# Kernel tuning notes

Measured on AMD Instinct MI355X. Metric: run time of the kernel, lower is better.

Reference implementation:

```python
import jax, jax.numpy as jnp
import numpy as np

DIM = 128
HEADS = 4
WIN = (2, 7, 7)
SHIFT = (1, 3, 3)
B, D, H, W = 8, 8, 56, 56
LN_EPS = 1e-5


def _rel_pos_index(ws):
    # static (N, N) int index into the relative position bias table
    coords = np.stack(np.meshgrid(np.arange(ws[0]), np.arange(ws[1]), np.arange(ws[2]), indexing='ij'))
    cf = coords.reshape(3, -1)
    rel = (cf[:, :, None] - cf[:, None, :]).transpose(1, 2, 0)  # (N, N, 3)
    rel[:, :, 0] += ws[0] - 1
    rel[:, :, 1] += ws[1] - 1
    rel[:, :, 2] += ws[2] - 1
    rel[:, :, 0] *= (2 * ws[1] - 1) * (2 * ws[2] - 1)
    rel[:, :, 1] *= 2 * ws[2] - 1
    return rel.sum(-1)


_REL_IDX = _rel_pos_index(WIN)  # (98, 98)


def _layernorm(x, g, b):
    m = x.mean(-1, keepdims=True)
    v = ((x - m) ** 2).mean(-1, keepdims=True)
    return (x - m) * jax.lax.rsqrt(v + LN_EPS) * g + b


def _forward(x, mask_matrix, norm1_g, norm1_b, qkv_w, qkv_b, rel_bias,
             proj_w, proj_b, norm2_g, norm2_b, fc1_w, fc1_b, fc2_w, fc2_b):
    Bx, Dx, Hx, Wx, C = x.shape
    wd, wh, ww = WIN
    sd, sh, sw = SHIFT
    N = wd * wh * ww
    hd = C // HEADS

    shortcut = x
    h = _layernorm(x, norm1_g, norm1_b)
    # cyclic shift (D, H, W divisible by window -> no padding needed)
    h = jnp.roll(h, (-sd, -sh, -sw), axis=(1, 2, 3))
    # window partition -> (B_, N, C)
    xw = h.reshape(Bx, Dx // wd, wd, Hx // wh, wh, Wx // ww, ww, C)
    xw = xw.transpose(0, 1, 3, 5, 2, 4, 6, 7).reshape(-1, N, C)
    B_ = xw.shape[0]

    qkv = xw @ qkv_w.T + qkv_b  # (B_, N, 3C)
    qkv = qkv.reshape(B_, N, 3, HEADS, hd).transpose(2, 0, 3, 1, 4)  # (3, B_, h, N, hd)
    q = qkv[0] * (hd ** -0.5)
    k = qkv[1]
    v = qkv[2]

    attn = jnp.einsum('bhnd,bhmd->bhnm', q, k)  # (B_, h, N, N)
    bias = rel_bias[_REL_IDX.reshape(-1)].reshape(N, N, HEADS).transpose(2, 0, 1)
    attn = attn + bias[None]
    nW = mask_matrix.shape[0]
    attn = attn.reshape(B_ // nW, nW, HEADS, N, N) + mask_matrix[None, :, None]
    attn = jax.nn.softmax(attn.reshape(B_, HEADS, N, N), axis=-1)

    out = jnp.einsum('bhnm,bhmd->bnhd', attn, v).reshape(B_, N, C)
    out = out @ proj_w.T + proj_b
    # window reverse -> (B, D, H, W, C)
    out = out.reshape(Bx, Dx // wd, Hx // wh, Wx // ww, wd, wh, ww, C)
    out = out.transpose(0, 1, 4, 2, 5, 3, 6, 7).reshape(Bx, Dx, Hx, Wx, C)
    out = jnp.roll(out, (sd, sh, sw), axis=(1, 2, 3))

    x = shortcut + out
    y = _layernorm(x, norm2_g, norm2_b)
    y = jax.nn.gelu(y @ fc1_w.T + fc1_b, approximate=False)
    y = y @ fc2_w.T + fc2_b
    return x + y


def setup_inputs():
    key = jax.random.key(0)
    ks = jax.random.split(key, 6)
    C = DIM
    wd, wh, ww = WIN
    x = jax.random.normal(ks[0], (B, D, H, W, C), jnp.float32)

    # shifted-window attention mask (standard Video-Swin compute_mask)
    img_mask = np.zeros((1, D, H, W, 1), np.float32)
    cnt = 0
    sl = lambda w, s: (slice(0, -w), slice(-w, -s), slice(-s, None))
    for d in sl(WIN[0], SHIFT[0]):
        for h in sl(WIN[1], SHIFT[1]):
            for w in sl(WIN[2], SHIFT[2]):
                img_mask[:, d, h, w, :] = cnt
                cnt += 1
    mw = img_mask.reshape(1, D // wd, wd, H // wh, wh, W // ww, ww, 1)
    mw = mw.transpose(0, 1, 3, 5, 2, 4, 6, 7).reshape(-1, wd * wh * ww)  # (nW, N)
    am = mw[:, None, :] - mw[:, :, None]
    mask_matrix = jnp.asarray(np.where(am != 0, -100.0, 0.0).astype(np.float32))

    nbias = (2 * wd - 1) * (2 * wh - 1) * (2 * ww - 1)
    p = lambda k, shape: jax.random.normal(k, shape, jnp.float32) * 0.02
    return {
        'x': x, 'mask_matrix': mask_matrix,
        'norm1_g': jnp.ones((C,), jnp.float32), 'norm1_b': jnp.zeros((C,), jnp.float32),
        'qkv_w': p(ks[1], (3 * C, C)), 'qkv_b': jnp.zeros((3 * C,), jnp.float32),
        'rel_bias': p(ks[2], (nbias, HEADS)),
        'proj_w': p(ks[3], (C, C)), 'proj_b': jnp.zeros((C,), jnp.float32),
        'norm2_g': jnp.ones((C,), jnp.float32), 'norm2_b': jnp.zeros((C,), jnp.float32),
        'fc1_w': p(ks[4], (4 * C, C)), 'fc1_b': jnp.zeros((4 * C,), jnp.float32),
        'fc2_w': p(ks[5], (C, 4 * C)), 'fc2_b': jnp.zeros((C,), jnp.float32),
    }


def reference(x, mask_matrix, norm1_g, norm1_b, qkv_w, qkv_b, rel_bias,
              proj_w, proj_b, norm2_g, norm2_b, fc1_w, fc1_b, fc2_w, fc2_b):
    return _forward(x, mask_matrix, norm1_g, norm1_b, qkv_w, qkv_b, rel_bias,
                    proj_w, proj_b, norm2_g, norm2_b, fc1_w, fc1_b, fc2_w, fc2_b)
```

## Files before the change

kernel.cpp:

```cpp
#include <hip/hip_runtime.h>
#include <hip/hip_bf16.h>

#define C_DIM 128
#define N_WIN 98
#define M_TOK 200704
#define B_WIN 2048

struct __align__(8) bf16x4 { __hip_bfloat16 h[4]; };

typedef __attribute__((ext_vector_type(8))) short bf16x8_t;
typedef __attribute__((ext_vector_type(4))) float f32x4_t;

__device__ __forceinline__ int token_spatial_index(int row) {
    int widx = row / 98;
    int n = row - widx * 98;
    int b   = widx >> 8;
    int rem = widx & 255;
    int dI = rem >> 6;
    int hI = (rem >> 3) & 7;
    int wI = rem & 7;
    int dw = n / 49;
    int r49 = n - dw * 49;
    int hw = r49 / 7;
    int ww = r49 - hw * 7;
    int d = dI * 2 + dw;
    int h = hI * 7 + hw;
    int w = wI * 7 + ww;
    d = (d + 1) & 7;
    h += 3; if (h >= 56) h -= 56;
    w += 3; if (w >= 56) w -= 56;
    return ((b * 8 + d) * 56 + h) * 56 + w;
}

__global__ __launch_bounds__(256) void ln1_qkv_kernel(
    const float* __restrict__ x,
    const float* __restrict__ g1,
    const float* __restrict__ b1,
    const float* __restrict__ qkv_w,
    const float* __restrict__ qkv_b,
    __hip_bfloat16* __restrict__ qkv_out)
{
    __shared__ __align__(16) __hip_bfloat16 Abf[64][136];
    __shared__ __align__(16) __hip_bfloat16 Wbf[192][136];
    __shared__ int srcL[64];

    const int tid  = threadIdx.x;
    const int lane = tid & 63;
    const int wv   = tid >> 6;
    const int rowbase = blockIdx.x * 64;

    if (tid < 64) srcL[tid] = token_spatial_index(rowbase + tid);
    __syncthreads();

    {
        int r = tid >> 2, part = tid & 3;
        const float* xp = x + (size_t)srcL[r] * 128 + part * 32;
        float v[32];
        float s = 0.f, ss = 0.f;
        #pragma unroll
        for (int j = 0; j < 8; ++j) {
            float4 f = *(const float4*)(xp + j * 4);
            v[j*4+0] = f.x; v[j*4+1] = f.y; v[j*4+2] = f.z; v[j*4+3] = f.w;
            s  += f.x + f.y + f.z + f.w;
            ss += f.x*f.x + f.y*f.y + f.z*f.z + f.w*f.w;
        }
        s += __shfl_xor(s, 1); ss += __shfl_xor(ss, 1);
        s += __shfl_xor(s, 2); ss += __shfl_xor(ss, 2);
        float m = s * (1.f / 128.f);
        float var = ss * (1.f / 128.f) - m * m;
        float rstd = rsqrtf(var + 1e-5f);
        #pragma unroll
        for (int j = 0; j < 8; ++j) {
            int k = part * 32 + j * 4;
            bf16x4 pk;
            pk.h[0] = __float2bfloat16((v[j*4+0] - m) * rstd * g1[k+0] + b1[k+0]);
            pk.h[1] = __float2bfloat16((v[j*4+1] - m) * rstd * g1[k+1] + b1[k+1]);
            pk.h[2] = __float2bfloat16((v[j*4+2] - m) * rstd * g1[k+2] + b1[k+2]);
            pk.h[3] = __float2bfloat16((v[j*4+3] - m) * rstd * g1[k+3] + b1[k+3]);
            *(bf16x4*)(&Abf[r][k]) = pk;
        }
    }
    __syncthreads();

    const int lm = lane & 15, quad = lane >> 4;
    const int rw = wv * 16;

    bf16x8_t xfr[4];
    #pragma unroll
    for (int s = 0; s < 4; ++s)
        xfr[s] = *(const bf16x8_t*)(&Abf[rw + lm][s * 32 + quad * 8]);

    for (int nt = 0; nt < 2; ++nt) {
        #pragma unroll
        for (int i = 0; i < 24; ++i) {
            int e = tid + i * 256;
            int c = e >> 5, kq = e & 31;
            float4 f = *(const float4*)(qkv_w + (size_t)(nt * 192 + c) * 128 + kq * 4);
            bf16x4 pk;
            pk.h[0] = __float2bfloat16(f.x); pk.h[1] = __float2bfloat16(f.y);
            pk.h[2] = __float2bfloat16(f.z); pk.h[3] = __float2bfloat16(f.w);
            *(bf16x4*)(&Wbf[c][kq * 4]) = pk;
        }
        __syncthreads();

        for (int ct = 0; ct < 12; ++ct) {
            f32x4_t acc = {0.f, 0.f, 0.f, 0.f};
            #pragma unroll
            for (int s = 0; s < 4; ++s) {
                bf16x8_t wfr = *(const bf16x8_t*)(&Wbf[ct * 16 + lm][s * 32 + quad * 8]);
                acc = __builtin_amdgcn_mfma_f32_16x16x32_bf16(wfr, xfr[s], acc, 0, 0, 0);
            }
            int grow = rowbase + rw + lm;
            int gcol = nt * 192 + ct * 16 + quad * 4;
            float4 bb = *(const float4*)(qkv_b + gcol);
            bf16x4 pk;
            pk.h[0] = __float2bfloat16(acc[0] + bb.x);
            pk.h[1] = __float2bfloat16(acc[1] + bb.y);
            pk.h[2] = __float2bfloat16(acc[2] + bb.z);
            pk.h[3] = __float2bfloat16(acc[3] + bb.w);
            *(bf16x4*)(qkv_out + (size_t)grow * 384 + gcol) = pk;
        }
        __syncthreads();
    }
}

__global__ __launch_bounds__(256) void attn_mfma_kernel(
    __hip_bfloat16* __restrict__ qkv,
    const float* __restrict__ rel_bias)
{
    __shared__ __align__(16) __hip_bfloat16 Qb[112][40];
    __shared__ __align__(16) __hip_bfloat16 Kb[112][40];
    __shared__ __align__(16) __hip_bfloat16 Vt[32][136];
    __shared__ __align__(16) __hip_bfloat16 Pb[112][136];
    __shared__ float biasL[507];
    __shared__ int   idn[98];

    const int tid  = threadIdx.x;
    const int lane = tid & 63;
    const int wv   = tid >> 6;
    const int widx = blockIdx.x >> 2;
    const int head = blockIdx.x & 3;
    const int co   = head * 32;
    const size_t base = (size_t)widx * 98 * 384;

    bf16x8_t zz = {};
    for (int e = tid; e < 448; e += 256) {
        int row = e >> 2, c8 = e & 3;
        if (row < 98) {
            size_t g = base + (size_t)row * 384;
            *(bf16x8_t*)(&Qb[row][c8 * 8]) = *(const bf16x8_t*)(qkv + g + co + c8 * 8);
            *(bf16x8_t*)(&Kb[row][c8 * 8]) = *(const bf16x8_t*)(qkv + g + 128 + co + c8 * 8);
        } else {
            *(bf16x8_t*)(&Qb[row][c8 * 8]) = zz;
            *(bf16x8_t*)(&Kb[row][c8 * 8]) = zz;
        }
    }
    for (int e = tid; e < 448; e += 256) {
        int row = e >> 2, c8 = e & 3;
        if (row < 98) {
            bf16x8_t v = *(const bf16x8_t*)(qkv + base + (size_t)row * 384 + 256 + co + c8 * 8);
            #pragma unroll
            for (int j = 0; j < 8; ++j) Vt[c8 * 8 + j][row] = ((__hip_bfloat16*)&v)[j];
        }
    }
    for (int e = tid; e < 1024; e += 256) {
        int r = e >> 5, c = 96 + (e & 31);
        if (c >= 98) Vt[r][c] = __float2bfloat16(0.f);
    }
    for (int e = tid; e < 1792; e += 256) {
        int r = e >> 4, c = 112 + (e & 15);
        Pb[r][c] = __float2bfloat16(0.f);
    }
    for (int i = tid; i < 507; i += 256) biasL[i] = rel_bias[i * 4 + head];
    if (tid < 98) {
        int wloc = widx & 255;
        int dI = wloc >> 6, hI = (wloc >> 3) & 7, wI = wloc & 7;
        int n = tid;
        int dw = n / 49, r49 = n - dw * 49, hw = r49 / 7, ww2 = r49 - hw * 7;
        int d = dI * 2 + dw, h = hI * 7 + hw, w = wI * 7 + ww2;
        int di = (d < 6) ? 0 : (d < 7 ? 1 : 2);
        int hi = (h < 49) ? 0 : (h < 52 ? 1 : 2);
        int wi = (w < 49) ? 0 : (w < 52 ? 1 : 2);
        idn[n] = di * 9 + hi * 3 + wi;
    }
    __syncthreads();

    const int lm = lane & 15, quad = lane >> 4;
    const float scale = 0.17677669529663687f;

    for (int tM = wv; tM < 7; tM += 4) {
        bf16x8_t afr = *(const bf16x8_t*)(&Qb[tM * 16 + lm][quad * 8]);
        f32x4_t acc[7];
        #pragma unroll
        for (int tN = 0; tN < 7; ++tN) {
            bf16x8_t bfr = *(const bf16x8_t*)(&Kb[tN * 16 + lm][quad * 8]);
            f32x4_t c0 = {0.f, 0.f, 0.f, 0.f};
            acc[tN] = __builtin_amdgcn_mfma_f32_16x16x32_bf16(afr, bfr, c0, 0, 0, 0);
        }
        float sv[7][4];
        #pragma unroll
        for (int tN = 0; tN < 7; ++tN) {
            int m = tN * 16 + lm;
            #pragma unroll
            for (int rg = 0; rg < 4; ++rg) {
                int n = tM * 16 + quad * 4 + rg;
                float s;
                if (n < 98 && m < 98) {
                    int d1 = n / 49, r1 = n - d1 * 49, h1 = r1 / 7, w1 = r1 - h1 * 7;
                    int d2 = m / 49, r2 = m - d2 * 49, h2 = r2 / 7, w2 = r2 - h2 * 7;
                    int bidx = (d1 - d2 + 1) * 169 + (h1 - h2 + 6) * 13 + (w1 - w2 + 6);
                    s = acc[tN][rg] * scale + biasL[bidx];
                    s += (idn[n] == idn[m]) ? 0.f : -100.f;
                } else {
                    s = -1e30f;
                }
                sv[tN][rg] = s;
            }
        }
        #pragma unroll
        for (int rg = 0; rg < 4; ++rg) {
            float mx = sv[0][rg];
            #pragma unroll
            for (int tN = 1; tN < 7; ++tN) mx = fmaxf(mx, sv[tN][rg]);
            mx = fmaxf(mx, __shfl_xor(mx, 1));
            mx = fmaxf(mx, __shfl_xor(mx, 2));
            mx = fmaxf(mx, __shfl_xor(mx, 4));
            mx = fmaxf(mx, __shfl_xor(mx, 8));
            float p[7], sum = 0.f;
            #pragma unroll
            for (int tN = 0; tN < 7; ++tN) { p[tN] = __expf(sv[tN][rg] - mx); sum += p[tN]; }
            sum += __shfl_xor(sum, 1);
            sum += __shfl_xor(sum, 2);
            sum += __shfl_xor(sum, 4);
            sum += __shfl_xor(sum, 8);
            float inv = 1.f / sum;
            int n = tM * 16 + quad * 4 + rg;
            #pragma unroll
            for (int tN = 0; tN < 7; ++tN)
                Pb[n][tN * 16 + lm] = __float2bfloat16(p[tN] * inv);
        }
    }
    __syncthreads();

    for (int t = wv; t < 14; t += 4) {
        int tM = t >> 1, tN = t & 1;
        f32x4_t acc = {0.f, 0.f, 0.f, 0.f};
        #pragma unroll
        for (int s = 0; s < 4; ++s) {
            bf16x8_t afr = *(const bf16x8_t*)(&Pb[tM * 16 + lm][s * 32 + quad * 8]);
            bf16x8_t bfr = *(const bf16x8_t*)(&Vt[tN * 16 + lm][s * 32 + quad * 8]);
            acc = __builtin_amdgcn_mfma_f32_16x16x32_bf16(afr, bfr, acc, 0, 0, 0);
        }
        int m = tN * 16 + lm;
        #pragma unroll
        for (int rg = 0; rg < 4; ++rg) {
            int n = tM * 16 + quad * 4 + rg;
            if (n < 98)
                qkv[base + (size_t)n * 384 + co + m] = __float2bfloat16(acc[rg]);
        }
    }
}

__global__ __launch_bounds__(256) void proj_kernel(
    const __hip_bfloat16* __restrict__ attn,
    const float* __restrict__ proj_w,
    const float* __restrict__ proj_b,
    const float* __restrict__ x,
    float* __restrict__ x2)
{
    __shared__ __align__(16) __hip_bfloat16 Abf[64][136];
    __shared__ __align__(16) __hip_bfloat16 Wbf[128][136];
    __shared__ int dstL[64];

    const int tid  = threadIdx.x;
    const int lane = tid & 63;
    const int wv   = tid >> 6;
    const int rowbase = blockIdx.x * 64;

    if (tid < 64) dstL[tid] = token_spatial_index(rowbase + tid);

    #pragma unroll
    for (int i = 0; i < 4; ++i) {
        int e = tid + i * 256;
        int r = e >> 4, c8 = e & 15;
        *(bf16x8_t*)(&Abf[r][c8 * 8]) = *(const bf16x8_t*)(attn + (size_t)(rowbase + r) * 384 + c8 * 8);
    }
    #pragma unroll
    for (int i = 0; i < 16; ++i) {
        int e = tid + i * 256;
        int c = e >> 5, kq = e & 31;
        float4 f = *(const float4*)(proj_w + (size_t)c * 128 + kq * 4);
        bf16x4 pk;
        pk.h[0] = __float2bfloat16(f.x); pk.h[1] = __float2bfloat16(f.y);
        pk.h[2] = __float2bfloat16(f.z); pk.h[3] = __float2bfloat16(f.w);
        *(bf16x4*)(&Wbf[c][kq * 4]) = pk;
    }
    __syncthreads();

    const int lm = lane & 15, quad = lane >> 4;
    const int rw = wv * 16;

    bf16x8_t xfr[4];
    #pragma unroll
    for (int s = 0; s < 4; ++s)
        xfr[s] = *(const bf16x8_t*)(&Abf[rw + lm][s * 32 + quad * 8]);

    const int dst = dstL[rw + lm];

    #pragma unroll
    for (int ct = 0; ct < 8; ++ct) {
        f32x4_t acc = {0.f, 0.f, 0.f, 0.f};
        #pragma unroll
        for (int s = 0; s < 4; ++s) {
            bf16x8_t wfr = *(const bf16x8_t*)(&Wbf[ct * 16 + lm][s * 32 + quad * 8]);
            acc = __builtin_amdgcn_mfma_f32_16x16x32_bf16(wfr, xfr[s], acc, 0, 0, 0);
        }
        int gcol = ct * 16 + quad * 4;
        float4 bb = *(const float4*)(proj_b + gcol);
        size_t off = (size_t)dst * 128 + gcol;
        float4 xr = *(const float4*)(x + off);
        float4 res;
        res.x = acc[0] + bb.x + xr.x;
        res.y = acc[1] + bb.y + xr.y;
        res.z = acc[2] + bb.z + xr.z;
        res.w = acc[3] + bb.w + xr.w;
        *(float4*)(x2 + off) = res;
    }
}

__global__ __launch_bounds__(256) void prep_weights(
    const float* __restrict__ fc1_w,
    const float* __restrict__ fc2_w,
    __hip_bfloat16* __restrict__ wb)
{
    int i = blockIdx.x * 256 + threadIdx.x;
    if (i < 65536)       wb[i] = __float2bfloat16(fc1_w[i]);
    else if (i < 131072) wb[i] = __float2bfloat16(fc2_w[i - 65536]);
}

__global__ __launch_bounds__(256, 3) void mlp_mfma_kernel(
    const float* __restrict__ x2,
    const float* __restrict__ g2,
    const float* __restrict__ b2,
    const __hip_bfloat16* __restrict__ fc1_wb,
    const __hip_bfloat16* __restrict__ fc2_wb,
    const float* __restrict__ fc1_b,
    const float* __restrict__ fc2_b,
    float* __restrict__ out)
{
    __shared__ __align__(16) __hip_bfloat16 Abf[64][136];
    __shared__ __align__(16) __hip_bfloat16 Hbf[64][264];

    const int tid  = threadIdx.x;
    const int lane = tid & 63;
    const int wv   = tid >> 6;
    const int rowbase = blockIdx.x * 64;

    {
        int r = tid >> 2, part = tid & 3;
        const float* xp = x2 + (size_t)(rowbase + r) * 128 + part * 32;
        float v[32];
        float s = 0.f, ss = 0.f;
        #pragma unroll
        for (int j = 0; j < 8; ++j) {
            float4 f = *(const float4*)(xp + j * 4);
            v[j*4+0] = f.x; v[j*4+1] = f.y; v[j*4+2] = f.z; v[j*4+3] = f.w;
            s  += f.x + f.y + f.z + f.w;
            ss += f.x*f.x + f.y*f.y + f.z*f.z + f.w*f.w;
        }
        s += __shfl_xor(s, 1); ss += __shfl_xor(ss, 1);
        s += __shfl_xor(s, 2); ss += __shfl_xor(ss, 2);
        float m = s * (1.f / 128.f);
        float var = ss * (1.f / 128.f) - m * m;
        float rstd = rsqrtf(var + 1e-5f);
        #pragma unroll
        for (int j = 0; j < 8; ++j) {
            int k = part * 32 + j * 4;
            bf16x4 pk;
            pk.h[0] = __float2bfloat16((v[j*4+0] - m) * rstd * g2[k+0] + b2[k+0]);
            pk.h[1] = __float2bfloat16((v[j*4+1] - m) * rstd * g2[k+1] + b2[k+1]);
            pk.h[2] = __float2bfloat16((v[j*4+2] - m) * rstd * g2[k+2] + b2[k+2]);
            pk.h[3] = __float2bfloat16((v[j*4+3] - m) * rstd * g2[k+3] + b2[k+3]);
            *(bf16x4*)(&Abf[r][k]) = pk;
        }
    }
    __syncthreads();

    const int lm   = lane & 15;
    const int quad = lane >> 4;

    f32x4_t acc2[2][4];
    #pragma unroll
    for (int ct = 0; ct < 2; ++ct)
        #pragma unroll
        for (int rt = 0; rt < 4; ++rt)
            acc2[ct][rt] = f32x4_t{0.f, 0.f, 0.f, 0.f};

    for (int c = 0; c < 2; ++c) {
        {
            bf16x8_t afr[4][4];
            #pragma unroll
            for (int rt = 0; rt < 4; ++rt)
                #pragma unroll
                for (int s = 0; s < 4; ++s)
                    afr[rt][s] = *(const bf16x8_t*)(&Abf[rt * 16 + lm][s * 32 + quad * 8]);

            #pragma unroll
            for (int ctb = 0; ctb < 2; ++ctb) {
                bf16x8_t wfr[2][4];
                #pragma unroll
                for (int cti = 0; cti < 2; ++cti) {
                    int hcol = c * 256 + wv * 64 + (ctb * 2 + cti) * 16 + lm;
                    const __hip_bfloat16* wp = fc1_wb + (size_t)hcol * 128 + quad * 8;
                    #pragma unroll
                    for (int s = 0; s < 4; ++s)
                        wfr[cti][s] = *(const bf16x8_t*)(wp + s * 32);
                }
                #pragma unroll
                for (int cti = 0; cti < 2; ++cti) {
                    int ct = ctb * 2 + cti;
                    int hcol = c * 256 + wv * 64 + ct * 16 + lm;
                    float bb = fc1_b[hcol];
                    f32x4_t a0 = {0.f,0.f,0.f,0.f}, a1 = {0.f,0.f,0.f,0.f};
                    f32x4_t a2 = {0.f,0.f,0.f,0.f}, a3 = {0.f,0.f,0.f,0.f};
                    #pragma unroll
                    for (int s = 0; s < 4; ++s) {
                        a0 = __builtin_amdgcn_mfma_f32_16x16x32_bf16(afr[0][s], wfr[cti][s], a0, 0, 0, 0);
                        a1 = __builtin_amdgcn_mfma_f32_16x16x32_bf16(afr[1][s], wfr[cti][s], a1, 0, 0, 0);
                        a2 = __builtin_amdgcn_mfma_f32_16x16x32_bf16(afr[2][s], wfr[cti][s], a2, 0, 0, 0);
                        a3 = __builtin_amdgcn_mfma_f32_16x16x32_bf16(afr[3][s], wfr[cti][s], a3, 0, 0, 0);
                    }
                    int lc = wv * 64 + ct * 16 + lm;
                    #pragma unroll
                    for (int rg = 0; rg < 4; ++rg) {
                        float v0 = a0[rg] + bb, v1 = a1[rg] + bb, v2 = a2[rg] + bb, v3 = a3[rg] + bb;
                        v0 = 0.5f * v0 * (1.f + erff(v0 * 0.70710678118654752f));
                        v1 = 0.5f * v1 * (1.f + erff(v1 * 0.70710678118654752f));
                        v2 = 0.5f * v2 * (1.f + erff(v2 * 0.70710678118654752f));
                        v3 = 0.5f * v3 * (1.f + erff(v3 * 0.70710678118654752f));
                        Hbf[ 0 + quad * 4 + rg][lc] = __float2bfloat16(v0);
                        Hbf[16 + quad * 4 + rg][lc] = __float2bfloat16(v1);
                        Hbf[32 + quad * 4 + rg][lc] = __float2bfloat16(v2);
                        Hbf[48 + quad * 4 + rg][lc] = __float2bfloat16(v3);
                    }
                }
            }
        }
        __syncthreads();

        {
            bf16x8_t wfr2[2][8];
            #pragma unroll
            for (int ct = 0; ct < 2; ++ct) {
                int ccol = wv * 32 + ct * 16 + lm;
                const __hip_bfloat16* wp = fc2_wb + (size_t)ccol * 512 + c * 256 + quad * 8;
                #pragma unroll
                for (int s = 0; s < 8; ++s)
                    wfr2[ct][s] = *(const bf16x8_t*)(wp + s * 32);
            }
            #pragma unroll
            for (int s = 0; s < 8; ++s) {
                bf16x8_t hfr[4];
                #pragma unroll
                for (int rt = 0; rt < 4; ++rt)
                    hfr[rt] = *(const bf16x8_t*)(&Hbf[rt * 16 + lm][s * 32 + quad * 8]);
                #pragma unroll
                for (int ct = 0; ct < 2; ++ct)
                    #pragma unroll
                    for (int rt = 0; rt < 4; ++rt)
                        acc2[ct][rt] = __builtin_amdgcn_mfma_f32_16x16x32_bf16(hfr[rt], wfr2[ct][s], acc2[ct][rt], 0, 0, 0);
            }
        }
        __syncthreads();
    }

    #pragma unroll
    for (int ct = 0; ct < 2; ++ct) {
        int ccol = wv * 32 + ct * 16 + lm;
        float bb = fc2_b[ccol];
        #pragma unroll
        for (int rt = 0; rt < 4; ++rt) {
            #pragma unroll
            for (int rg = 0; rg < 4; ++rg) {
                int rr = rt * 16 + quad * 4 + rg;
                size_t off = (size_t)(rowbase + rr) * 128 + ccol;
                out[off] = acc2[ct][rt][rg] + bb + x2[off];
            }
        }
    }
}

extern "C" void kernel_launch(void* const* d_in, const int* in_sizes, int n_in,
                              void* d_out, int out_size, void* d_ws, size_t ws_size,
                              hipStream_t stream) {
    const float* x        = (const float*)d_in[0];
    const float* n1g      = (const float*)d_in[2];
    const float* n1b      = (const float*)d_in[3];
    const float* qkv_w    = (const float*)d_in[4];
    const float* qkv_b    = (const float*)d_in[5];
    const float* rel_bias = (const float*)d_in[6];
    const float* proj_w   = (const float*)d_in[7];
    const float* proj_b   = (const float*)d_in[8];
    const float* n2g      = (const float*)d_in[9];
    const float* n2b      = (const float*)d_in[10];
    const float* fc1_w    = (const float*)d_in[11];
    const float* fc1_b    = (const float*)d_in[12];
    const float* fc2_w    = (const float*)d_in[13];
    const float* fc2_b    = (const float*)d_in[14];
    float* out = (float*)d_out;

    __hip_bfloat16* qkv = (__hip_bfloat16*)d_ws;
    float* x2 = (float*)((char*)d_ws + 154140672);
    __hip_bfloat16* wb  = (__hip_bfloat16*)d_ws;
    __hip_bfloat16* fc1_wb = wb;
    __hip_bfloat16* fc2_wb = wb + 65536;

    ln1_qkv_kernel<<<3136, 256, 0, stream>>>(x, n1g, n1b, qkv_w, qkv_b, qkv);
    attn_mfma_kernel<<<8192, 256, 0, stream>>>(qkv, rel_bias);
    proj_kernel<<<3136, 256, 0, stream>>>(qkv, proj_w, proj_b, x, x2);
    prep_weights<<<512, 256, 0, stream>>>(fc1_w, fc2_w, wb);
    mlp_mfma_kernel<<<3136, 256, 0, stream>>>(x2, n2g, n2b, fc1_wb, fc2_wb, fc1_b, fc2_b, out);
}
```

Before: 682.3 us.

## Swizzle attention LDS tiles, load Q directly, precompute bias indices

Swaps the padded shared-memory layouts of the P and transposed-V tiles for XOR-swizzled 128-wide rows, which is meant to cut LDS bank conflicts without the padding. Q fragments are now read straight from global memory into registers, so the Q shared tile and its staging pass go away. The per-element div/mod arithmetic for the relative-position bias index is replaced by per-token offsets precomputed into shared memory, and the per-column offsets and mask ids are hoisted into registers. This raises register pressure, and the direct Q loads are uncoalesced global reads.

```diff
diff --git a/kernel.cpp b/kernel.cpp
--- a/kernel.cpp
+++ b/kernel.cpp
@@ -124,16 +124,18 @@
     }
 }
 
+#define SWZ(r, c) (((r) * 128) + ((c) ^ (((r) & 7) << 3)))
+
 __global__ __launch_bounds__(256) void attn_mfma_kernel(
     __hip_bfloat16* __restrict__ qkv,
     const float* __restrict__ rel_bias)
 {
-    __shared__ __align__(16) __hip_bfloat16 Qb[112][40];
     __shared__ __align__(16) __hip_bfloat16 Kb[112][40];
-    __shared__ __align__(16) __hip_bfloat16 Vt[32][136];
-    __shared__ __align__(16) __hip_bfloat16 Pb[112][136];
+    __shared__ __align__(16) __hip_bfloat16 Vt[32 * 128];
+    __shared__ __align__(16) __hip_bfloat16 Pb[112 * 128];
     __shared__ float biasL[507];
-    __shared__ int   idn[98];
+    __shared__ int   idnL[98];
+    __shared__ int   nbL[98];
 
     const int tid  = threadIdx.x;
     const int lane = tid & 63;
@@ -147,11 +149,9 @@
     for (int e = tid; e < 448; e += 256) {
         int row = e >> 2, c8 = e & 3;
         if (row < 98) {
-            size_t g = base + (size_t)row * 384;
-            *(bf16x8_t*)(&Qb[row][c8 * 8]) = *(const bf16x8_t*)(qkv + g + co + c8 * 8);
-            *(bf16x8_t*)(&Kb[row][c8 * 8]) = *(const bf16x8_t*)(qkv + g + 128 + co + c8 * 8);
+            *(bf16x8_t*)(&Kb[row][c8 * 8]) =
+                *(const bf16x8_t*)(qkv + base + (size_t)row * 384 + 128 + co + c8 * 8);
         } else {
-            *(bf16x8_t*)(&Qb[row][c8 * 8]) = zz;
             *(bf16x8_t*)(&Kb[row][c8 * 8]) = zz;
         }
     }
@@ -160,36 +160,50 @@
         if (row < 98) {
             bf16x8_t v = *(const bf16x8_t*)(qkv + base + (size_t)row * 384 + 256 + co + c8 * 8);
             #pragma unroll
-            for (int j = 0; j < 8; ++j) Vt[c8 * 8 + j][row] = ((__hip_bfloat16*)&v)[j];
+            for (int j = 0; j < 8; ++j) Vt[SWZ(c8 * 8 + j, row)] = ((__hip_bfloat16*)&v)[j];
         }
     }
     for (int e = tid; e < 1024; e += 256) {
         int r = e >> 5, c = 96 + (e & 31);
-        if (c >= 98) Vt[r][c] = __float2bfloat16(0.f);
+        if (c >= 98) Vt[SWZ(r, c)] = __float2bfloat16(0.f);
     }
     for (int e = tid; e < 1792; e += 256) {
         int r = e >> 4, c = 112 + (e & 15);
-        Pb[r][c] = __float2bfloat16(0.f);
+        Pb[SWZ(r, c)] = __float2bfloat16(0.f);
     }
     for (int i = tid; i < 507; i += 256) biasL[i] = rel_bias[i * 4 + head];
     if (tid < 98) {
+        int n = tid;
+        int dw = n / 49, r49 = n - dw * 49, hw = r49 / 7, ww2 = r49 - hw * 7;
+        nbL[n] = dw * 169 + hw * 13 + ww2;
         int wloc = widx & 255;
         int dI = wloc >> 6, hI = (wloc >> 3) & 7, wI = wloc & 7;
-        int n = tid;
-        int dw = n / 49, r49 = n - dw * 49, hw = r49 / 7, ww2 = r49 - hw * 7;
         int d = dI * 2 + dw, h = hI * 7 + hw, w = wI * 7 + ww2;
         int di = (d < 6) ? 0 : (d < 7 ? 1 : 2);
         int hi = (h < 49) ? 0 : (h < 52 ? 1 : 2);
         int wi = (w < 49) ? 0 : (w < 52 ? 1 : 2);
-        idn[n] = di * 9 + hi * 3 + wi;
+        idnL[n] = di * 9 + hi * 3 + wi;
     }
     __syncthreads();
 
     const int lm = lane & 15, quad = lane >> 4;
     const float scale = 0.17677669529663687f;
 
+    int  mnb[7], mid[7];
+    bool mok[7];
+    #pragma unroll
+    for (int tN = 0; tN < 7; ++tN) {
+        int m = tN * 16 + lm;
+        mok[tN] = (m < 98);
+        mnb[tN] = mok[tN] ? nbL[m] : 0;
+        mid[tN] = mok[tN] ? idnL[m] : -1;
+    }
+
     for (int tM = wv; tM < 7; tM += 4) {
-        bf16x8_t afr = *(const bf16x8_t*)(&Qb[tM * 16 + lm][quad * 8]);
+        int qrow = tM * 16 + lm;
+        bf16x8_t afr = zz;
+        if (qrow < 98)
+            afr = *(const bf16x8_t*)(qkv + base + (size_t)qrow * 384 + co + quad * 8);
         f32x4_t acc[7];
         #pragma unroll
         for (int tN = 0; tN < 7; ++tN) {
@@ -197,20 +211,24 @@
             f32x4_t c0 = {0.f, 0.f, 0.f, 0.f};
             acc[tN] = __builtin_amdgcn_mfma_f32_16x16x32_bf16(afr, bfr, c0, 0, 0, 0);
         }
+        int  nnb[4], nid[4];
+        bool nok[4];
+        #pragma unroll
+        for (int rg = 0; rg < 4; ++rg) {
+            int n = tM * 16 + quad * 4 + rg;
+            nok[rg] = (n < 98);
+            nnb[rg] = nok[rg] ? nbL[n] : 0;
+            nid[rg] = nok[rg] ? idnL[n] : -2;
+        }
         float sv[7][4];
         #pragma unroll
         for (int tN = 0; tN < 7; ++tN) {
-            int m = tN * 16 + lm;
             #pragma unroll
             for (int rg = 0; rg < 4; ++rg) {
-                int n = tM * 16 + quad * 4 + rg;
                 float s;
-                if (n < 98 && m < 98) {
-                    int d1 = n / 49, r1 = n - d1 * 49, h1 = r1 / 7, w1 = r1 - h1 * 7;
-                    int d2 = m / 49, r2 = m - d2 * 49, h2 = r2 / 7, w2 = r2 - h2 * 7;
-                    int bidx = (d1 - d2 + 1) * 169 + (h1 - h2 + 6) * 13 + (w1 - w2 + 6);
-                    s = acc[tN][rg] * scale + biasL[bidx];
-                    s += (idn[n] == idn[m]) ? 0.f : -100.f;
+                if (nok[rg] && mok[tN]) {
+                    s = acc[tN][rg] * scale + biasL[nnb[rg] - mnb[tN] + 253];
+                    s += (nid[rg] == mid[tN]) ? 0.f : -100.f;
                 } else {
                     s = -1e30f;
                 }
@@ -237,7 +255,7 @@
             int n = tM * 16 + quad * 4 + rg;
             #pragma unroll
             for (int tN = 0; tN < 7; ++tN)
-                Pb[n][tN * 16 + lm] = __float2bfloat16(p[tN] * inv);
+                Pb[SWZ(n, tN * 16 + lm)] = __float2bfloat16(p[tN] * inv);
         }
     }
     __syncthreads();
@@ -247,8 +265,8 @@
         f32x4_t acc = {0.f, 0.f, 0.f, 0.f};
         #pragma unroll
         for (int s = 0; s < 4; ++s) {
-            bf16x8_t afr = *(const bf16x8_t*)(&Pb[tM * 16 + lm][s * 32 + quad * 8]);
-            bf16x8_t bfr = *(const bf16x8_t*)(&Vt[tN * 16 + lm][s * 32 + quad * 8]);
+            bf16x8_t afr = *(const bf16x8_t*)(&Pb[SWZ(tM * 16 + lm, s * 32 + quad * 8)]);
+            bf16x8_t bfr = *(const bf16x8_t*)(&Vt[SWZ(tN * 16 + lm, s * 32 + quad * 8)]);
             acc = __builtin_amdgcn_mfma_f32_16x16x32_bf16(afr, bfr, acc, 0, 0, 0);
         }
         int m = tN * 16 + lm;
```

After: 611.5 us. 10.4% less time.
